# Kernel tuning notes

Hardware: AMD Instinct MI355X
Metric: run time of the kernel (lower is better)

Reference implementation:

```python
import jax, jax.numpy as jnp
import numpy as np

N_NODES = 200000
N_EDGES = 3200000
N_GRAPHS = 64
IN_DIM, HIDDEN, OUT_DIM = 128, 16, 64


def setup_inputs() -> dict:
    key = jax.random.key(0)
    ks = jax.random.split(key, 5)
    x = jax.random.normal(ks[0], (N_NODES, IN_DIM), dtype=jnp.float32)
    edge_index = jax.random.randint(ks[1], (2, N_EDGES), 0, N_NODES, dtype=jnp.int64)
    batch = jnp.sort(jax.random.randint(ks[2], (N_NODES,), 0, N_GRAPHS, dtype=jnp.int64))
    W1 = jax.random.normal(ks[3], (IN_DIM, HIDDEN), dtype=jnp.float32) * (1.0 / np.sqrt(IN_DIM))
    W2 = jax.random.normal(ks[4], (HIDDEN, OUT_DIM), dtype=jnp.float32) * (1.0 / np.sqrt(HIDDEN))
    b1 = jnp.zeros((HIDDEN,), jnp.float32)
    b2 = jnp.zeros((OUT_DIM,), jnp.float32)
    return {"x": x, "edge_index": edge_index, "batch": batch,
            "W1": W1, "b1": b1, "W2": W2, "b2": b2, "training": 0}


def _gcn_conv(x, W, b, row, col, n_nodes):
    # PyG GCNConv: add-self-loop symmetric normalization, transform then
    # gather-from-row / scatter-add-to-col.  (row, col) already include self-loops.
    h = x @ W                                             # [N, out]
    deg = jnp.zeros((n_nodes,), h.dtype).at[col].add(1.0)  # degree incl. self-loop (>=1)
    dinv = deg ** -0.5
    norm = dinv[row] * dinv[col]                          # [E+N]
    out = jnp.zeros((n_nodes, W.shape[1]), h.dtype).at[col].add(h[row] * norm[:, None])
    return out + b


def reference(x, edge_index, batch, W1, b1, W2, b2, training):
    n = x.shape[0]
    loops = jnp.arange(n, dtype=edge_index.dtype)
    row = jnp.concatenate([edge_index[0], loops])
    col = jnp.concatenate([edge_index[1], loops])
    h = _gcn_conv(x, W1, b1, row, col, n)
    h = jax.nn.relu(h)
    # F.dropout with training=False is identity (reference is deterministic)
    h = _gcn_conv(h, W2, b2, row, col, n)
    # per-graph sum pooling: replaces the Python torch.where loop
    graph_embeds = jax.ops.segment_sum(h, batch, num_segments=N_GRAPHS)
    return graph_embeds
```

## Files before the change

### kernel.cpp

```cpp
#include <hip/hip_runtime.h>


#define TPB 256
#define CHUNK 4096
#define BK_SHIFT 10
#define NPB 1024

__device__ __forceinline__ float bf2f(unsigned short u) {
    union { unsigned int i; float f; } v; v.i = ((unsigned int)u) << 16; return v.f;
}
__device__ __forceinline__ unsigned short f2bf(float f) {
    union { float f; unsigned int i; } v; v.f = f;
    unsigned int r = v.i + 0x7fff + ((v.i >> 16) & 1);
    return (unsigned short)(r >> 16);
}

__global__ __launch_bounds__(TPB) void hist_kernel(const int* __restrict__ col,
                                                   int* __restrict__ counts,
                                                   int E, int nblk, int nbuck) {
    __shared__ int hist[256];
    int t = threadIdx.x;
    if (t < nbuck) hist[t] = 0;
    __syncthreads();
    int e0 = blockIdx.x * CHUNK;
    for (int i = t; i < CHUNK; i += TPB) {
        int e = e0 + i;
        if (e < E) atomicAdd(&hist[col[e] >> BK_SHIFT], 1);
    }
    __syncthreads();
    if (t < nbuck) counts[t * nblk + blockIdx.x] = hist[t];
}

__global__ __launch_bounds__(TPB) void scan1_kernel(const int* __restrict__ in,
                                                    int* __restrict__ out,
                                                    int* __restrict__ bsum, int L) {
    __shared__ int s[TPB];
    int t = threadIdx.x;
    int i = blockIdx.x * TPB + t;
    int d = (i < L) ? in[i] : 0;
    s[t] = d; __syncthreads();
    for (int off = 1; off < TPB; off <<= 1) {
        int v = (t >= off) ? s[t - off] : 0;
        __syncthreads();
        s[t] += v;
        __syncthreads();
    }
    if (i < L) out[i] = s[t] - d;
    if (t == TPB - 1) bsum[blockIdx.x] = s[t];
}

__global__ __launch_bounds__(1024) void scan2_kernel(int* __restrict__ bsum, int nb) {
    __shared__ int s[1024];
    int t = threadIdx.x;
    int v = (t < nb) ? bsum[t] : 0;
    s[t] = v; __syncthreads();
    for (int off = 1; off < 1024; off <<= 1) {
        int u = (t >= off) ? s[t - off] : 0;
        __syncthreads();
        s[t] += u;
        __syncthreads();
    }
    if (t < nb) bsum[t] = s[t] - v;
}

__global__ __launch_bounds__(TPB) void scan3g_kernel(int* __restrict__ out,
                                                     const int* __restrict__ bsum, int L) {
    int i = blockIdx.x * TPB + threadIdx.x;
    if (i < L) out[i] += bsum[blockIdx.x];
}

__global__ __launch_bounds__(TPB) void s1c_gemm_kernel(
        const int* __restrict__ row, const int* __restrict__ col,
        const int* __restrict__ cbase, int E, int nblk, int nbuck,
        int2* __restrict__ bucketed,
        const float* __restrict__ x, const float* __restrict__ W1,
        float* __restrict__ h1, int N, int nbg) {
    __shared__ int cur[256];
    __shared__ float w1s[128 * 16];
    int b = (int)blockIdx.x, t = threadIdx.x;
    int M = min(nblk, nbg);
    int role, id;
    if (b < 2 * M) { role = b & 1; id = b >> 1; }
    else           { role = (nblk > nbg) ? 0 : 1; id = b - M; }

    if (role == 0) {
        if (t < nbuck) cur[t] = cbase[t * nblk + id];
        __syncthreads();
        int e0 = id * CHUNK;
        for (int i = t; i < CHUNK; i += TPB) {
            int e = e0 + i;
            if (e < E) {
                int c = col[e];
                int pos = atomicAdd(&cur[c >> BK_SHIFT], 1);
                bucketed[pos] = make_int2(c, row[e]);
            }
        }
        return;
    }
    for (int i = t; i < 128 * 16; i += TPB) w1s[i] = W1[i];
    __syncthreads();
    int n = id * TPB + t;
    if (n >= N) return;
    const float4* xr = (const float4*)(x + (size_t)n * 128);
    float acc[16];
#pragma unroll
    for (int k = 0; k < 16; ++k) acc[k] = 0.f;
#pragma unroll 1
    for (int g = 0; g < 8; ++g) {
        float4 v0 = xr[g * 4 + 0], v1 = xr[g * 4 + 1];
        float4 v2 = xr[g * 4 + 2], v3 = xr[g * 4 + 3];
        float xv[16] = {v0.x, v0.y, v0.z, v0.w, v1.x, v1.y, v1.z, v1.w,
                        v2.x, v2.y, v2.z, v2.w, v3.x, v3.y, v3.z, v3.w};
#pragma unroll
        for (int cc = 0; cc < 16; ++cc) {
            const float4* w4 = (const float4*)&w1s[(g * 16 + cc) * 16];
            float4 wa = w4[0], wb = w4[1], wc = w4[2], wd = w4[3];
            float xc = xv[cc];
            acc[0]  = fmaf(xc, wa.x, acc[0]);  acc[1]  = fmaf(xc, wa.y, acc[1]);
            acc[2]  = fmaf(xc, wa.z, acc[2]);  acc[3]  = fmaf(xc, wa.w, acc[3]);
            acc[4]  = fmaf(xc, wb.x, acc[4]);  acc[5]  = fmaf(xc, wb.y, acc[5]);
            acc[6]  = fmaf(xc, wb.z, acc[6]);  acc[7]  = fmaf(xc, wb.w, acc[7]);
            acc[8]  = fmaf(xc, wc.x, acc[8]);  acc[9]  = fmaf(xc, wc.y, acc[9]);
            acc[10] = fmaf(xc, wc.z, acc[10]); acc[11] = fmaf(xc, wc.w, acc[11]);
            acc[12] = fmaf(xc, wd.x, acc[12]); acc[13] = fmaf(xc, wd.y, acc[13]);
            acc[14] = fmaf(xc, wd.z, acc[14]); acc[15] = fmaf(xc, wd.w, acc[15]);
        }
    }
    float4* o = (float4*)(h1 + (size_t)n * 16);
    o[0] = make_float4(acc[0], acc[1], acc[2], acc[3]);
    o[1] = make_float4(acc[4], acc[5], acc[6], acc[7]);
    o[2] = make_float4(acc[8], acc[9], acc[10], acc[11]);
    o[3] = make_float4(acc[12], acc[13], acc[14], acc[15]);
}

__global__ __launch_bounds__(TPB) void sort_kernel(
        const int2* __restrict__ bucketed, const int* __restrict__ cbase,
        int E, int nblk, int nbuck,
        int* __restrict__ csr, int* __restrict__ offs, float* __restrict__ dinv,
        const float* __restrict__ h1, unsigned short* __restrict__ h1p, int N) {
    __shared__ int lhist[NPB];
    __shared__ int part[TPB];
    __shared__ float sdinv[NPB];
    int bk = blockIdx.x, t = threadIdx.x;
    int n0 = bk << BK_SHIFT;
    int n1 = min(n0 + NPB, N);
    int e0 = cbase[bk * nblk];
    int e1 = (bk + 1 < nbuck) ? cbase[(bk + 1) * nblk] : E;

    for (int i = t; i < NPB; i += TPB) lhist[i] = 0;
    __syncthreads();
    for (int i = e0 + t; i < e1; i += TPB)
        atomicAdd(&lhist[bucketed[i].x & (NPB - 1)], 1);
    __syncthreads();

    int base = t * 4;
    int c0 = lhist[base], c1 = lhist[base + 1], c2 = lhist[base + 2], c3 = lhist[base + 3];
    int s = c0 + c1 + c2 + c3;
    part[t] = s;
    __syncthreads();
    for (int off = 1; off < TPB; off <<= 1) {
        int v = (t >= off) ? part[t - off] : 0;
        __syncthreads();
        part[t] += v;
        __syncthreads();
    }
    int o0 = e0 + part[t] - s;
    int o1 = o0 + c0, o2 = o1 + c1, o3 = o2 + c2;
    lhist[base] = o0; lhist[base + 1] = o1; lhist[base + 2] = o2; lhist[base + 3] = o3;
    sdinv[base]     = rsqrtf((float)c0 + 1.0f);
    sdinv[base + 1] = rsqrtf((float)c1 + 1.0f);
    sdinv[base + 2] = rsqrtf((float)c2 + 1.0f);
    sdinv[base + 3] = rsqrtf((float)c3 + 1.0f);
    int n = n0 + base;
    if (n + 0 < N) { offs[n + 0] = o0; dinv[n + 0] = sdinv[base]; }
    if (n + 1 < N) { offs[n + 1] = o1; dinv[n + 1] = sdinv[base + 1]; }
    if (n + 2 < N) { offs[n + 2] = o2; dinv[n + 2] = sdinv[base + 2]; }
    if (n + 3 < N) { offs[n + 3] = o3; dinv[n + 3] = sdinv[base + 3]; }
    __syncthreads();

    for (int i = e0 + t; i < e1; i += TPB) {
        int2 cr = bucketed[i];
        int pos = atomicAdd(&lhist[cr.x & (NPB - 1)], 1);
        csr[pos] = cr.y;
    }
    int nq = (n1 - n0) * 4;
    for (int i = t; i < nq; i += TPB) {
        float dv = sdinv[i >> 2];
        float4 v = ((const float4*)h1)[(size_t)n0 * 4 + i];
        ((ushort4*)h1p)[(size_t)n0 * 4 + i] =
            make_ushort4(f2bf(v.x * dv), f2bf(v.y * dv), f2bf(v.z * dv), f2bf(v.w * dv));
    }
    if (bk == 0 && t == 0) offs[N] = E;
}

__global__ __launch_bounds__(TPB) void gather1_kernel(const int* __restrict__ csr,
                                                      const int* __restrict__ offs,
                                                      const unsigned short* __restrict__ h1p,
                                                      const float* __restrict__ dinv,
                                                      const float* __restrict__ b1,
                                                      unsigned short* __restrict__ h2p, int N) {
    int t = threadIdx.x;
    int c = blockIdx.x * 16 + (t >> 4);
    int k = t & 15;
    if (c >= N) return;
    int p0 = offs[c], p1 = offs[c + 1];
    float acc = 0.f;
    for (int p = p0; p < p1; p += 16) {
        int idx = p + k;
        int s = csr[min(idx, p1 - 1)];
        int rem = p1 - p;
        float v[16];
#pragma unroll
        for (int j = 0; j < 16; ++j) {
            int sj = __shfl(s, j, 16);
            v[j] = bf2f(h1p[(size_t)sj * 16 + k]);
        }
#pragma unroll
        for (int j = 0; j < 16; ++j) acc += (j < rem) ? v[j] : 0.f;
    }
    float dc = dinv[c];
    float self = bf2f(h1p[(size_t)c * 16 + k]);
    float a = fmaf(dc, acc + self, b1[k]);
    h2p[(size_t)c * 16 + k] = f2bf(dc * fmaxf(a, 0.f));
}

__global__ __launch_bounds__(TPB) void gather2_kernel(const int* __restrict__ csr,
                                                      const int* __restrict__ offs,
                                                      const unsigned short* __restrict__ h2p,
                                                      const float* __restrict__ dinv,
                                                      float* __restrict__ a2, int N) {
    int t = threadIdx.x;
    int c = blockIdx.x * 16 + (t >> 4);
    int k = t & 15;
    if (c >= N) return;
    int p0 = offs[c], p1 = offs[c + 1];
    float acc = 0.f;
    for (int p = p0; p < p1; p += 16) {
        int idx = p + k;
        int s = csr[min(idx, p1 - 1)];
        int rem = p1 - p;
        float v[16];
#pragma unroll
        for (int j = 0; j < 16; ++j) {
            int sj = __shfl(s, j, 16);
            v[j] = bf2f(h2p[(size_t)sj * 16 + k]);
        }
#pragma unroll
        for (int j = 0; j < 16; ++j) acc += (j < rem) ? v[j] : 0.f;
    }
    float self = bf2f(h2p[(size_t)c * 16 + k]);
    a2[(size_t)c * 16 + k] = dinv[c] * (acc + self);
}

__global__ __launch_bounds__(TPB) void final_kernel(const float* __restrict__ a2,
                                                    const float* __restrict__ W2,
                                                    const float* __restrict__ b2,
                                                    const int* __restrict__ batch,
                                                    float* __restrict__ out, int N) {
    __shared__ float w2s[16 * 64];
    int t = threadIdx.x;
    for (int i = t; i < 16 * 64; i += TPB) w2s[i] = W2[i];
    __syncthreads();

    int wave = t >> 6, lane = t & 63;
    int n0 = blockIdx.x * 256 + wave * 64;
    float b2k = b2[lane];
    int g_cur = -1;
    float acc = 0.f;
    for (int i = 0; i < 64; ++i) {
        int n = n0 + i;
        if (n >= N) break;
        const float* ar = a2 + (size_t)n * 16;
        float val = b2k;
#pragma unroll
        for (int j = 0; j < 16; ++j) val = fmaf(ar[j], w2s[j * 64 + lane], val);
        int g = batch[n];
        if (g != g_cur) {
            if (g_cur >= 0) atomicAdd(&out[(size_t)g_cur * 64 + lane], acc);
            acc = 0.f;
            g_cur = g;
        }
        acc += val;
    }
    if (g_cur >= 0) atomicAdd(&out[(size_t)g_cur * 64 + lane], acc);
}

static inline size_t align64(size_t v) { return (v + 63) & ~(size_t)63; }

extern "C" void kernel_launch(void* const* d_in, const int* in_sizes, int n_in,
                              void* d_out, int out_size, void* d_ws, size_t ws_size,
                              hipStream_t stream) {
    const float* x     = (const float*)d_in[0];
    const int*   ei    = (const int*)d_in[1];
    const int*   batch = (const int*)d_in[2];
    const float* W1    = (const float*)d_in[3];
    const float* b1    = (const float*)d_in[4];
    const float* W2    = (const float*)d_in[5];
    const float* b2    = (const float*)d_in[6];

    const int N = in_sizes[0] / 128;
    const int E = in_sizes[1] / 2;
    const int* row = ei;
    const int* col = ei + E;

    const int NBLK  = (E + CHUNK - 1) / CHUNK;
    const int NBUCK = (N + NPB - 1) / NPB;
    const int L     = NBUCK * NBLK;
    const int NBS   = (L + TPB - 1) / TPB;
    const int NBG   = (N + TPB - 1) / TPB;

    char* p = (char*)d_ws;
    int*            counts   = (int*)p;            p += align64((size_t)L * 4);
    int*            bsum     = (int*)p;            p += align64(1024 * 4);
    int2*           bucketed = (int2*)p;           p += align64((size_t)E * 8);
    int*            csr      = (int*)p;            p += align64((size_t)E * 4);
    int*            offs     = (int*)p;            p += align64((size_t)(N + 1) * 4);
    float*          dinv     = (float*)p;          p += align64((size_t)N * 4);
    float*          h1       = (float*)p;          p += align64((size_t)N * 16 * 4);
    unsigned short* h1p      = (unsigned short*)p; p += align64((size_t)N * 16 * 2);
    unsigned short* h2p      = (unsigned short*)p; p += align64((size_t)N * 16 * 2);
    float*          a2       = h1;
    float*          out      = (float*)d_out;

    hipMemsetAsync(out, 0, (size_t)out_size * sizeof(float), stream);

    hist_kernel<<<NBLK, TPB, 0, stream>>>(col, counts, E, NBLK, NBUCK);
    scan1_kernel<<<NBS, TPB, 0, stream>>>(counts, counts, bsum, L);
    scan2_kernel<<<1, 1024, 0, stream>>>(bsum, NBS);
    scan3g_kernel<<<NBS, TPB, 0, stream>>>(counts, bsum, L);
    s1c_gemm_kernel<<<NBLK + NBG, TPB, 0, stream>>>(row, col, counts, E, NBLK, NBUCK,
                                                    bucketed, x, W1, h1, N, NBG);
    sort_kernel<<<NBUCK, TPB, 0, stream>>>(bucketed, counts, E, NBLK, NBUCK,
                                           csr, offs, dinv, h1, h1p, N);
    gather1_kernel<<<(N + 15) / 16, TPB, 0, stream>>>(csr, offs, h1p, dinv, b1, h2p, N);
    gather2_kernel<<<(N + 15) / 16, TPB, 0, stream>>>(csr, offs, h2p, dinv, a2, N);
    final_kernel<<<(N + 255) / 256, TPB, 0, stream>>>(a2, W2, b2, batch, out, N);
}
```

Measured before the change: 398.9 us.

## Pack bucketed edges into 32-bit, shrink buckets, stage x in LDS, widen gathers

Edges are bucketed as a single packed 32-bit word (local column in the high bits, source row in the low 18 bits) instead of an int2, which halves the traffic of the bucketed array. Bucket size drops to 512 nodes and the edge chunk doubles, so the histogram arrays grow to 512 entries. The x@W1 GEMM now loads x cooperatively through padded shared memory and reads W1 straight from global memory. Each gather kernel now gives one full 64-lane wave to a destination node, with four neighbours per step and a shuffle reduction, trading more idle lanes on low-degree nodes for more loads in flight. The 18-bit row packing only works while N stays at or below 262144.

```diff
diff --git a/kernel.cpp b/kernel.cpp
--- a/kernel.cpp
+++ b/kernel.cpp
@@ -2,9 +2,9 @@
 
 
 #define TPB 256
-#define CHUNK 4096
-#define BK_SHIFT 10
-#define NPB 1024
+#define CHUNK 8192
+#define BK_SHIFT 9
+#define NPB 512
 
 __device__ __forceinline__ float bf2f(unsigned short u) {
     union { unsigned int i; float f; } v; v.i = ((unsigned int)u) << 16; return v.f;
@@ -18,9 +18,9 @@
 __global__ __launch_bounds__(TPB) void hist_kernel(const int* __restrict__ col,
                                                    int* __restrict__ counts,
                                                    int E, int nblk, int nbuck) {
-    __shared__ int hist[256];
-    int t = threadIdx.x;
-    if (t < nbuck) hist[t] = 0;
+    __shared__ int hist[512];
+    int t = threadIdx.x;
+    for (int i = t; i < nbuck; i += TPB) hist[i] = 0;
     __syncthreads();
     int e0 = blockIdx.x * CHUNK;
     for (int i = t; i < CHUNK; i += TPB) {
@@ -28,7 +28,7 @@
         if (e < E) atomicAdd(&hist[col[e] >> BK_SHIFT], 1);
     }
     __syncthreads();
-    if (t < nbuck) counts[t * nblk + blockIdx.x] = hist[t];
+    for (int i = t; i < nbuck; i += TPB) counts[i * nblk + blockIdx.x] = hist[i];
 }
 
 __global__ __launch_bounds__(TPB) void scan1_kernel(const int* __restrict__ in,
@@ -72,11 +72,10 @@
 __global__ __launch_bounds__(TPB) void s1c_gemm_kernel(
         const int* __restrict__ row, const int* __restrict__ col,
         const int* __restrict__ cbase, int E, int nblk, int nbuck,
-        int2* __restrict__ bucketed,
+        int* __restrict__ bucketed,
         const float* __restrict__ x, const float* __restrict__ W1,
         float* __restrict__ h1, int N, int nbg) {
-    __shared__ int cur[256];
-    __shared__ float w1s[128 * 16];
+    __shared__ float smem[256 * 17];
     int b = (int)blockIdx.x, t = threadIdx.x;
     int M = min(nblk, nbg);
     int role, id;
@@ -84,7 +83,8 @@
     else           { role = (nblk > nbg) ? 0 : 1; id = b - M; }
 
     if (role == 0) {
-        if (t < nbuck) cur[t] = cbase[t * nblk + id];
+        int* cur = (int*)smem;
+        for (int i = t; i < nbuck; i += TPB) cur[i] = cbase[i * nblk + id];
         __syncthreads();
         int e0 = id * CHUNK;
         for (int i = t; i < CHUNK; i += TPB) {
@@ -92,49 +92,58 @@
             if (e < E) {
                 int c = col[e];
                 int pos = atomicAdd(&cur[c >> BK_SHIFT], 1);
-                bucketed[pos] = make_int2(c, row[e]);
+                bucketed[pos] = ((c & (NPB - 1)) << 18) | row[e];
             }
         }
         return;
     }
-    for (int i = t; i < 128 * 16; i += TPB) w1s[i] = W1[i];
-    __syncthreads();
-    int n = id * TPB + t;
-    if (n >= N) return;
-    const float4* xr = (const float4*)(x + (size_t)n * 128);
+    float* xs = smem;
+    int n0 = id * TPB;
+    int n = n0 + t;
+    int nrows = min(TPB, N - n0);
     float acc[16];
 #pragma unroll
     for (int k = 0; k < 16; ++k) acc[k] = 0.f;
 #pragma unroll 1
-    for (int g = 0; g < 8; ++g) {
-        float4 v0 = xr[g * 4 + 0], v1 = xr[g * 4 + 1];
-        float4 v2 = xr[g * 4 + 2], v3 = xr[g * 4 + 3];
-        float xv[16] = {v0.x, v0.y, v0.z, v0.w, v1.x, v1.y, v1.z, v1.w,
-                        v2.x, v2.y, v2.z, v2.w, v3.x, v3.y, v3.z, v3.w};
-#pragma unroll
-        for (int cc = 0; cc < 16; ++cc) {
-            const float4* w4 = (const float4*)&w1s[(g * 16 + cc) * 16];
-            float4 wa = w4[0], wb = w4[1], wc = w4[2], wd = w4[3];
-            float xc = xv[cc];
-            acc[0]  = fmaf(xc, wa.x, acc[0]);  acc[1]  = fmaf(xc, wa.y, acc[1]);
-            acc[2]  = fmaf(xc, wa.z, acc[2]);  acc[3]  = fmaf(xc, wa.w, acc[3]);
-            acc[4]  = fmaf(xc, wb.x, acc[4]);  acc[5]  = fmaf(xc, wb.y, acc[5]);
-            acc[6]  = fmaf(xc, wb.z, acc[6]);  acc[7]  = fmaf(xc, wb.w, acc[7]);
-            acc[8]  = fmaf(xc, wc.x, acc[8]);  acc[9]  = fmaf(xc, wc.y, acc[9]);
-            acc[10] = fmaf(xc, wc.z, acc[10]); acc[11] = fmaf(xc, wc.w, acc[11]);
-            acc[12] = fmaf(xc, wd.x, acc[12]); acc[13] = fmaf(xc, wd.y, acc[13]);
-            acc[14] = fmaf(xc, wd.z, acc[14]); acc[15] = fmaf(xc, wd.w, acc[15]);
-        }
-    }
-    float4* o = (float4*)(h1 + (size_t)n * 16);
-    o[0] = make_float4(acc[0], acc[1], acc[2], acc[3]);
-    o[1] = make_float4(acc[4], acc[5], acc[6], acc[7]);
-    o[2] = make_float4(acc[8], acc[9], acc[10], acc[11]);
-    o[3] = make_float4(acc[12], acc[13], acc[14], acc[15]);
+    for (int ch = 0; ch < 8; ++ch) {
+        __syncthreads();
+        for (int f = t; f < nrows * 4; f += TPB) {
+            int r = f >> 2, q = f & 3;
+            const float* src = x + (size_t)(n0 + r) * 128 + ch * 16 + q * 4;
+            float4 v = *(const float4*)src;
+            float* dst = &xs[r * 17 + q * 4];
+            dst[0] = v.x; dst[1] = v.y; dst[2] = v.z; dst[3] = v.w;
+        }
+        __syncthreads();
+        if (n < N) {
+            const float* xr = &xs[t * 17];
+#pragma unroll
+            for (int c = 0; c < 16; ++c) {
+                float xc = xr[c];
+                const float4* w4 = (const float4*)(W1 + (size_t)(ch * 16 + c) * 16);
+                float4 wa = w4[0], wb = w4[1], wc = w4[2], wd = w4[3];
+                acc[0]  = fmaf(xc, wa.x, acc[0]);  acc[1]  = fmaf(xc, wa.y, acc[1]);
+                acc[2]  = fmaf(xc, wa.z, acc[2]);  acc[3]  = fmaf(xc, wa.w, acc[3]);
+                acc[4]  = fmaf(xc, wb.x, acc[4]);  acc[5]  = fmaf(xc, wb.y, acc[5]);
+                acc[6]  = fmaf(xc, wb.z, acc[6]);  acc[7]  = fmaf(xc, wb.w, acc[7]);
+                acc[8]  = fmaf(xc, wc.x, acc[8]);  acc[9]  = fmaf(xc, wc.y, acc[9]);
+                acc[10] = fmaf(xc, wc.z, acc[10]); acc[11] = fmaf(xc, wc.w, acc[11]);
+                acc[12] = fmaf(xc, wd.x, acc[12]); acc[13] = fmaf(xc, wd.y, acc[13]);
+                acc[14] = fmaf(xc, wd.z, acc[14]); acc[15] = fmaf(xc, wd.w, acc[15]);
+            }
+        }
+    }
+    if (n < N) {
+        float4* o = (float4*)(h1 + (size_t)n * 16);
+        o[0] = make_float4(acc[0], acc[1], acc[2], acc[3]);
+        o[1] = make_float4(acc[4], acc[5], acc[6], acc[7]);
+        o[2] = make_float4(acc[8], acc[9], acc[10], acc[11]);
+        o[3] = make_float4(acc[12], acc[13], acc[14], acc[15]);
+    }
 }
 
 __global__ __launch_bounds__(TPB) void sort_kernel(
-        const int2* __restrict__ bucketed, const int* __restrict__ cbase,
+        const int* __restrict__ bucketed, const int* __restrict__ cbase,
         int E, int nblk, int nbuck,
         int* __restrict__ csr, int* __restrict__ offs, float* __restrict__ dinv,
         const float* __restrict__ h1, unsigned short* __restrict__ h1p, int N) {
@@ -147,15 +156,15 @@
     int e0 = cbase[bk * nblk];
     int e1 = (bk + 1 < nbuck) ? cbase[(bk + 1) * nblk] : E;
 
-    for (int i = t; i < NPB; i += TPB) lhist[i] = 0;
+    lhist[t] = 0; lhist[t + TPB] = 0;
     __syncthreads();
     for (int i = e0 + t; i < e1; i += TPB)
-        atomicAdd(&lhist[bucketed[i].x & (NPB - 1)], 1);
-    __syncthreads();
-
-    int base = t * 4;
-    int c0 = lhist[base], c1 = lhist[base + 1], c2 = lhist[base + 2], c3 = lhist[base + 3];
-    int s = c0 + c1 + c2 + c3;
+        atomicAdd(&lhist[bucketed[i] >> 18], 1);
+    __syncthreads();
+
+    int base = t * 2;
+    int c0 = lhist[base], c1 = lhist[base + 1];
+    int s = c0 + c1;
     part[t] = s;
     __syncthreads();
     for (int off = 1; off < TPB; off <<= 1) {
@@ -165,23 +174,19 @@
         __syncthreads();
     }
     int o0 = e0 + part[t] - s;
-    int o1 = o0 + c0, o2 = o1 + c1, o3 = o2 + c2;
-    lhist[base] = o0; lhist[base + 1] = o1; lhist[base + 2] = o2; lhist[base + 3] = o3;
+    int o1 = o0 + c0;
+    lhist[base] = o0; lhist[base + 1] = o1;
     sdinv[base]     = rsqrtf((float)c0 + 1.0f);
     sdinv[base + 1] = rsqrtf((float)c1 + 1.0f);
-    sdinv[base + 2] = rsqrtf((float)c2 + 1.0f);
-    sdinv[base + 3] = rsqrtf((float)c3 + 1.0f);
     int n = n0 + base;
     if (n + 0 < N) { offs[n + 0] = o0; dinv[n + 0] = sdinv[base]; }
     if (n + 1 < N) { offs[n + 1] = o1; dinv[n + 1] = sdinv[base + 1]; }
-    if (n + 2 < N) { offs[n + 2] = o2; dinv[n + 2] = sdinv[base + 2]; }
-    if (n + 3 < N) { offs[n + 3] = o3; dinv[n + 3] = sdinv[base + 3]; }
     __syncthreads();
 
     for (int i = e0 + t; i < e1; i += TPB) {
-        int2 cr = bucketed[i];
-        int pos = atomicAdd(&lhist[cr.x & (NPB - 1)], 1);
-        csr[pos] = cr.y;
+        int v = bucketed[i];
+        int pos = atomicAdd(&lhist[v >> 18], 1);
+        csr[pos] = v & 0x3FFFF;
     }
     int nq = (n1 - n0) * 4;
     for (int i = t; i < nq; i += TPB) {
@@ -200,28 +205,32 @@
                                                       const float* __restrict__ b1,
                                                       unsigned short* __restrict__ h2p, int N) {
     int t = threadIdx.x;
-    int c = blockIdx.x * 16 + (t >> 4);
-    int k = t & 15;
+    int c = blockIdx.x * 4 + (t >> 6);
+    int lane = t & 63;
+    int k = lane & 15, sub = lane >> 4;
     if (c >= N) return;
     int p0 = offs[c], p1 = offs[c + 1];
     float acc = 0.f;
     for (int p = p0; p < p1; p += 16) {
-        int idx = p + k;
-        int s = csr[min(idx, p1 - 1)];
         int rem = p1 - p;
-        float v[16];
-#pragma unroll
-        for (int j = 0; j < 16; ++j) {
-            int sj = __shfl(s, j, 16);
-            v[j] = bf2f(h1p[(size_t)sj * 16 + k]);
-        }
-#pragma unroll
-        for (int j = 0; j < 16; ++j) acc += (j < rem) ? v[j] : 0.f;
-    }
-    float dc = dinv[c];
-    float self = bf2f(h1p[(size_t)c * 16 + k]);
-    float a = fmaf(dc, acc + self, b1[k]);
-    h2p[(size_t)c * 16 + k] = f2bf(dc * fmaxf(a, 0.f));
+        float v[4];
+#pragma unroll
+        for (int u = 0; u < 4; ++u) {
+            int idx = p + u * 4 + sub;
+            int sidx = csr[min(idx, p1 - 1)];
+            v[u] = bf2f(h1p[(size_t)sidx * 16 + k]);
+        }
+#pragma unroll
+        for (int u = 0; u < 4; ++u) acc += (u * 4 + sub < rem) ? v[u] : 0.f;
+    }
+    acc += __shfl_down(acc, 32);
+    acc += __shfl_down(acc, 16);
+    if (sub == 0) {
+        float dc = dinv[c];
+        float self = bf2f(h1p[(size_t)c * 16 + k]);
+        float a = fmaf(dc, acc + self, b1[k]);
+        h2p[(size_t)c * 16 + k] = f2bf(dc * fmaxf(a, 0.f));
+    }
 }
 
 __global__ __launch_bounds__(TPB) void gather2_kernel(const int* __restrict__ csr,
@@ -230,26 +239,30 @@
                                                       const float* __restrict__ dinv,
                                                       float* __restrict__ a2, int N) {
     int t = threadIdx.x;
-    int c = blockIdx.x * 16 + (t >> 4);
-    int k = t & 15;
+    int c = blockIdx.x * 4 + (t >> 6);
+    int lane = t & 63;
+    int k = lane & 15, sub = lane >> 4;
     if (c >= N) return;
     int p0 = offs[c], p1 = offs[c + 1];
     float acc = 0.f;
     for (int p = p0; p < p1; p += 16) {
-        int idx = p + k;
-        int s = csr[min(idx, p1 - 1)];
         int rem = p1 - p;
-        float v[16];
-#pragma unroll
-        for (int j = 0; j < 16; ++j) {
-            int sj = __shfl(s, j, 16);
-            v[j] = bf2f(h2p[(size_t)sj * 16 + k]);
-        }
-#pragma unroll
-        for (int j = 0; j < 16; ++j) acc += (j < rem) ? v[j] : 0.f;
-    }
-    float self = bf2f(h2p[(size_t)c * 16 + k]);
-    a2[(size_t)c * 16 + k] = dinv[c] * (acc + self);
+        float v[4];
+#pragma unroll
+        for (int u = 0; u < 4; ++u) {
+            int idx = p + u * 4 + sub;
+            int sidx = csr[min(idx, p1 - 1)];
+            v[u] = bf2f(h2p[(size_t)sidx * 16 + k]);
+        }
+#pragma unroll
+        for (int u = 0; u < 4; ++u) acc += (u * 4 + sub < rem) ? v[u] : 0.f;
+    }
+    acc += __shfl_down(acc, 32);
+    acc += __shfl_down(acc, 16);
+    if (sub == 0) {
+        float self = bf2f(h2p[(size_t)c * 16 + k]);
+        a2[(size_t)c * 16 + k] = dinv[c] * (acc + self);
+    }
 }
 
 __global__ __launch_bounds__(TPB) void final_kernel(const float* __restrict__ a2,
@@ -312,7 +325,7 @@
     char* p = (char*)d_ws;
     int*            counts   = (int*)p;            p += align64((size_t)L * 4);
     int*            bsum     = (int*)p;            p += align64(1024 * 4);
-    int2*           bucketed = (int2*)p;           p += align64((size_t)E * 8);
+    int*            bucketed = (int*)p;            p += align64((size_t)E * 4);
     int*            csr      = (int*)p;            p += align64((size_t)E * 4);
     int*            offs     = (int*)p;            p += align64((size_t)(N + 1) * 4);
     float*          dinv     = (float*)p;          p += align64((size_t)N * 4);
@@ -332,7 +345,7 @@
                                                     bucketed, x, W1, h1, N, NBG);
     sort_kernel<<<NBUCK, TPB, 0, stream>>>(bucketed, counts, E, NBLK, NBUCK,
                                            csr, offs, dinv, h1, h1p, N);
-    gather1_kernel<<<(N + 15) / 16, TPB, 0, stream>>>(csr, offs, h1p, dinv, b1, h2p, N);
-    gather2_kernel<<<(N + 15) / 16, TPB, 0, stream>>>(csr, offs, h2p, dinv, a2, N);
+    gather1_kernel<<<(N + 3) / 4, TPB, 0, stream>>>(csr, offs, h1p, dinv, b1, h2p, N);
+    gather2_kernel<<<(N + 3) / 4, TPB, 0, stream>>>(csr, offs, h2p, dinv, a2, N);
     final_kernel<<<(N + 255) / 256, TPB, 0, stream>>>(a2, W2, b2, batch, out, N);
 }
```

Measured after the change: 465.7 us. 1.17x slower.
